# Optimization experiments

Measured on AMD Instinct MI355X. Metric: run time of the kernel, lower is better.

The kernel has to match this reference:

```python
import jax, jax.numpy as jnp
import numpy as np

I, H, O = 3, 16, 5
B, S = 4096, 512


def setup_inputs() -> dict:
    key = jax.random.key(0)
    ks = jax.random.split(key, 4)
    scale = 0.1  # xavier gain=0.1 ballpark; exact init irrelevant for correctness baseline
    return {
        "x": jax.random.normal(ks[0], (B, S, I), dtype=jnp.float32),
        "W_ih": jax.random.normal(ks[1], (4 * H, I), dtype=jnp.float32) * scale,
        "W_hh": jax.random.normal(ks[2], (4 * H, H), dtype=jnp.float32) * scale,
        "b_ih": jnp.zeros((4 * H,), dtype=jnp.float32),
        "b_hh": jnp.zeros((4 * H,), dtype=jnp.float32),
        "W_lin": jax.random.normal(ks[3], (O, H), dtype=jnp.float32) * scale,
        "b_lin": jnp.zeros((O,), dtype=jnp.float32),
    }


def _lstm(x, W_ih, W_hh, b_ih, b_hh):
    # Precompute input contribution for all timesteps: [B, S, 4H]
    xg = jnp.einsum('bsi,gi->bsg', x, W_ih) + b_ih + b_hh
    xg = jnp.swapaxes(xg, 0, 1)  # [S, B, 4H] for scan
    h0 = jnp.zeros((x.shape[0], H), dtype=x.dtype)
    c0 = jnp.zeros_like(h0)

    def step(carry, xt):
        h, c = carry
        gates = xt + h @ W_hh.T  # [B, 4H]
        i, f, g, o = jnp.split(gates, 4, axis=-1)  # PyTorch gate order i,f,g,o
        i = jax.nn.sigmoid(i)
        f = jax.nn.sigmoid(f)
        g = jnp.tanh(g)
        o = jax.nn.sigmoid(o)
        c = f * c + i * g
        h = o * jnp.tanh(c)
        return (h, c), h

    _, hs = jax.lax.scan(step, (h0, c0), xg)
    return jnp.swapaxes(hs, 0, 1)  # [B, S, H]


def reference(x, W_ih, W_hh, b_ih, b_hh, W_lin, b_lin):
    out1 = _lstm(x, W_ih, W_hh, b_ih, b_hh)            # [B, S, H]
    out = jnp.einsum('bsh,oh->bso', out1, W_lin) + b_lin  # [B, S, O]
    return jnp.clip(out, -10.0, 10.0)
```

## Files before the change

### kernel.cpp

```cpp
#include <hip/hip_runtime.h>


#define TS 512
#define LOG2E 1.44269504088896340736f

typedef float f32x2 __attribute__((ext_vector_type(2)));

#define BCAST(K) hbr[K] = __int_as_float( \
    __builtin_amdgcn_update_dpp(0, hvi, 0x150 + (K), 0xf, 0xf, true))
#define BCAST_ALL() \
  BCAST(0); BCAST(1); BCAST(2); BCAST(3); BCAST(4); BCAST(5); BCAST(6); BCAST(7); \
  BCAST(8); BCAST(9); BCAST(10); BCAST(11); BCAST(12); BCAST(13); BCAST(14); BCAST(15)

__global__ __launch_bounds__(256)
__attribute__((amdgpu_waves_per_eu(1, 1)))
void lstm_enc_kernel(const float* __restrict__ x,
                     const float* __restrict__ W_ih,
                     const float* __restrict__ W_hh,
                     const float* __restrict__ b_ih,
                     const float* __restrict__ b_hh,
                     const float* __restrict__ W_lin,
                     const float* __restrict__ b_lin,
                     float* __restrict__ out) {
  const int tid = threadIdx.x;
  const int j = tid & 15;
  const int g = tid >> 4;
  const int batch = blockIdx.x * 16 + g;
  const int jo = (j < 5) ? j : 0;

  __shared__ float4 xs[2][64][16];
  float4* xsf = &xs[0][0][0];

  f32x2 wif[16], wgo[16];
  float wl[16];
#pragma unroll
  for (int k = 0; k < 16; ++k) {
    wif[k] = f32x2{W_hh[(j     ) * 16 + k] * LOG2E,
                   W_hh[(j + 16) * 16 + k] * LOG2E};
    wgo[k] = f32x2{W_hh[(j + 32) * 16 + k] * (2.0f * LOG2E),
                   W_hh[(j + 48) * 16 + k] * LOG2E};
    wl[k]  = W_lin[jo * 16 + k];
  }
  f32x2 xw[3], xwg[3];
#pragma unroll
  for (int i = 0; i < 3; ++i) {
    xw[i]  = f32x2{W_ih[(j     ) * 3 + i] * LOG2E,
                   W_ih[(j + 16) * 3 + i] * LOG2E};
    xwg[i] = f32x2{W_ih[(j + 32) * 3 + i] * (2.0f * LOG2E),
                   W_ih[(j + 48) * 3 + i] * LOG2E};
  }
  const f32x2 bif = f32x2{(b_ih[j     ] + b_hh[j     ]) * LOG2E,
                          (b_ih[j + 16] + b_hh[j + 16]) * LOG2E};
  const f32x2 bgo = f32x2{(b_ih[j + 32] + b_hh[j + 32]) * (2.0f * LOG2E),
                          (b_ih[j + 48] + b_hh[j + 48]) * LOG2E};
  const float bl = b_lin[jo];

  const float* __restrict__ xb = x + (size_t)batch * (TS * 3);
  float* __restrict__ ob = out + (size_t)batch * (TS * 5) + j;
  const bool storer = (j < 5);

  const float* xc0 = xb + j * 12;
  float4 q0, q1, q2;

  q0 = *(const float4*)(xc0 + 0);
  q1 = *(const float4*)(xc0 + 4);
  q2 = *(const float4*)(xc0 + 8);
  {
    const int wb = j * 4 * 16 + g;
    xsf[wb +  0] = float4{q0.x, q0.y, q0.z, 0.f};
    xsf[wb + 16] = float4{q0.w, q1.x, q1.y, 0.f};
    xsf[wb + 32] = float4{q1.z, q1.w, q2.x, 0.f};
    xsf[wb + 48] = float4{q2.y, q2.z, q2.w, 0.f};
  }
  q0 = *(const float4*)(xc0 + 192 + 0);
  q1 = *(const float4*)(xc0 + 192 + 4);
  q2 = *(const float4*)(xc0 + 192 + 8);

  float4 xr[2];
  xr[0] = xsf[0 * 16 + g];
  xr[1] = xsf[1 * 16 + g];

  float h = 0.0f, c = 0.0f;

  auto step = [&](int s, int slot) {
    const float4 xt = xr[slot];
    xr[slot] = xsf[(((s + 2) & 127) << 4) + g];

    float hbr[16];
    const int hvi = __float_as_int(h);
    BCAST_ALL();

    f32x2 aa = bif, ab = f32x2{0.f, 0.f};
    f32x2 ga = bgo, gb = f32x2{0.f, 0.f};
    float oa0 = bl, oa1 = 0.f;
    aa = f32x2{xt.x, xt.x} * xw[0] + aa;
    ab = f32x2{xt.y, xt.y} * xw[1] + ab;
    aa = f32x2{xt.z, xt.z} * xw[2] + aa;
    ga = f32x2{xt.x, xt.x} * xwg[0] + ga;
    gb = f32x2{xt.y, xt.y} * xwg[1] + gb;
    ga = f32x2{xt.z, xt.z} * xwg[2] + ga;
#pragma unroll
    for (int k = 0; k < 16; k += 2) {
      const f32x2 h0 = f32x2{hbr[k], hbr[k]};
      const f32x2 h1 = f32x2{hbr[k + 1], hbr[k + 1]};
      aa = h0 * wif[k] + aa;
      ab = h1 * wif[k + 1] + ab;
      ga = h0 * wgo[k] + ga;
      gb = h1 * wgo[k + 1] + gb;
      oa0 = fmaf(hbr[k], wl[k], oa0);
      oa1 = fmaf(hbr[k + 1], wl[k + 1], oa1);
    }
    const f32x2 zif = aa + ab;
    const f32x2 zgo = ga + gb;

    if (s > 0 && storer) {
      const float oa = oa0 + oa1;
      ob[(s - 1) * 5] = fminf(fmaxf(oa, -10.0f), 10.0f);
    }

    const float ig = __builtin_amdgcn_rcpf(1.0f + __builtin_amdgcn_exp2f(-zif.x));
    const float fg = __builtin_amdgcn_rcpf(1.0f + __builtin_amdgcn_exp2f(-zif.y));
    const float sg = __builtin_amdgcn_rcpf(1.0f + __builtin_amdgcn_exp2f(zgo.x));
    const float og = __builtin_amdgcn_rcpf(1.0f + __builtin_amdgcn_exp2f(-zgo.y));

    const float gg = fmaf(-2.0f, sg, 1.0f);
    c = fmaf(fg, c, ig * gg);
    const float tc = fmaf(-2.0f,
        __builtin_amdgcn_rcpf(1.0f + __builtin_amdgcn_exp2f((2.0f * LOG2E) * c)), 1.0f);
    h = og * tc;
  };

  for (int ch = 0; ch < 8; ++ch) {
    const int base = ch * 64;

#pragma unroll 2
    for (int u = 0; u < 32; ++u) step(base + u, u & 1);

    if (ch < 7) {
      const int p = (ch + 1) & 1;
      const int wb = p * 1024 + j * 64 + g;
      xsf[wb +  0] = float4{q0.x, q0.y, q0.z, 0.f};
      xsf[wb + 16] = float4{q0.w, q1.x, q1.y, 0.f};
      xsf[wb + 32] = float4{q1.z, q1.w, q2.x, 0.f};
      xsf[wb + 48] = float4{q2.y, q2.z, q2.w, 0.f};
    }
    if (ch < 6) {
      const float* xc = xc0 + (ch + 2) * 192;
      q0 = *(const float4*)(xc + 0);
      q1 = *(const float4*)(xc + 4);
      q2 = *(const float4*)(xc + 8);
    }

#pragma unroll 2
    for (int u = 32; u < 64; ++u) step(base + u, u & 1);
  }

  {
    float hbr[16];
    const int hvi = __float_as_int(h);
    BCAST_ALL();
    float oa = bl;
#pragma unroll
    for (int k = 0; k < 16; ++k) oa = fmaf(hbr[k], wl[k], oa);
    if (storer) {
      ob[(TS - 1) * 5] = fminf(fmaxf(oa, -10.0f), 10.0f);
    }
  }
}

extern "C" void kernel_launch(void* const* d_in, const int* in_sizes, int n_in,
                              void* d_out, int out_size, void* d_ws, size_t ws_size,
                              hipStream_t stream) {
  const float* x     = (const float*)d_in[0];
  const float* W_ih  = (const float*)d_in[1];
  const float* W_hh  = (const float*)d_in[2];
  const float* b_ih  = (const float*)d_in[3];
  const float* b_hh  = (const float*)d_in[4];
  const float* W_lin = (const float*)d_in[5];
  const float* b_lin = (const float*)d_in[6];
  float* out = (float*)d_out;

  const int B = in_sizes[0] / (TS * 3);
  const int grid = B / 16;
  lstm_enc_kernel<<<grid, 256, 0, stream>>>(x, W_ih, W_hh, b_ih, b_hh, W_lin, b_lin, out);
}
```

Baseline: 212.5 us.

## Compute LSTM recurrent gates with split-bf16 MFMA instead of DPP-broadcast FMAs

Replaces the per-lane DPP broadcast of h and scalar packed FMAs with 16x16x32 bf16 MFMA instructions. Each weight and activation is split into hi and lo bf16 parts and three MFMA passes approximate fp32 accuracy. The input projection and the output linear layer are folded into the same matrix product by appending x to the K dimension. Gate results and h are exchanged through per-wave LDS buffers each step. This adds LDS round trips and MFMA latency to the serial recurrence critical path, and precision is only roughly fp32.

```diff
diff --git a/kernel.cpp b/kernel.cpp
--- a/kernel.cpp
+++ b/kernel.cpp
@@ -4,13 +4,15 @@
 #define TS 512
 #define LOG2E 1.44269504088896340736f
 
-typedef float f32x2 __attribute__((ext_vector_type(2)));
-
-#define BCAST(K) hbr[K] = __int_as_float( \
-    __builtin_amdgcn_update_dpp(0, hvi, 0x150 + (K), 0xf, 0xf, true))
-#define BCAST_ALL() \
-  BCAST(0); BCAST(1); BCAST(2); BCAST(3); BCAST(4); BCAST(5); BCAST(6); BCAST(7); \
-  BCAST(8); BCAST(9); BCAST(10); BCAST(11); BCAST(12); BCAST(13); BCAST(14); BCAST(15)
+typedef float f32x4 __attribute__((ext_vector_type(4)));
+typedef short s16x8 __attribute__((ext_vector_type(8)));
+typedef unsigned int u32;
+typedef u32 u32x4 __attribute__((ext_vector_type(4)));
+typedef f32x4 f32x4u __attribute__((aligned(4)));
+
+static __device__ __forceinline__ float clip10(float v) {
+  return fminf(fmaxf(v, -10.0f), 10.0f);
+}
 
 __global__ __launch_bounds__(256)
 __attribute__((amdgpu_waves_per_eu(1, 1)))
@@ -23,147 +25,231 @@
                      const float* __restrict__ b_lin,
                      float* __restrict__ out) {
   const int tid = threadIdx.x;
-  const int j = tid & 15;
-  const int g = tid >> 4;
-  const int batch = blockIdx.x * 16 + g;
-  const int jo = (j < 5) ? j : 0;
+  const int w   = tid >> 6;
+  const int q   = (tid >> 4) & 3;
+  const int col = tid & 15;
+  const int g16 = tid >> 4;
 
   __shared__ float4 xs[2][64][16];
+  __shared__ f32x4  zbuf[4][4][20];
+  __shared__ __attribute__((aligned(16))) u32 hbuf[4][4][36];
+
   float4* xsf = &xs[0][0][0];
-
-  f32x2 wif[16], wgo[16];
-  float wl[16];
-#pragma unroll
-  for (int k = 0; k < 16; ++k) {
-    wif[k] = f32x2{W_hh[(j     ) * 16 + k] * LOG2E,
-                   W_hh[(j + 16) * 16 + k] * LOG2E};
-    wgo[k] = f32x2{W_hh[(j + 32) * 16 + k] * (2.0f * LOG2E),
-                   W_hh[(j + 48) * 16 + k] * LOG2E};
-    wl[k]  = W_lin[jo * 16 + k];
-  }
-  f32x2 xw[3], xwg[3];
-#pragma unroll
-  for (int i = 0; i < 3; ++i) {
-    xw[i]  = f32x2{W_ih[(j     ) * 3 + i] * LOG2E,
-                   W_ih[(j + 16) * 3 + i] * LOG2E};
-    xwg[i] = f32x2{W_ih[(j + 32) * 3 + i] * (2.0f * LOG2E),
-                   W_ih[(j + 48) * 3 + i] * LOG2E};
-  }
-  const f32x2 bif = f32x2{(b_ih[j     ] + b_hh[j     ]) * LOG2E,
-                          (b_ih[j + 16] + b_hh[j + 16]) * LOG2E};
-  const f32x2 bgo = f32x2{(b_ih[j + 32] + b_hh[j + 32]) * (2.0f * LOG2E),
-                          (b_ih[j + 48] + b_hh[j + 48]) * LOG2E};
-  const float bl = b_lin[jo];
-
-  const float* __restrict__ xb = x + (size_t)batch * (TS * 3);
-  float* __restrict__ ob = out + (size_t)batch * (TS * 5) + j;
-  const bool storer = (j < 5);
-
-  const float* xc0 = xb + j * 12;
-  float4 q0, q1, q2;
-
-  q0 = *(const float4*)(xc0 + 0);
-  q1 = *(const float4*)(xc0 + 4);
-  q2 = *(const float4*)(xc0 + 8);
+  float*  zf  = (float*)&zbuf[w][0][0];
+  u32*    hb  = &hbuf[w][0][0];
+
+  s16x8 a_hi[4], a_lo[4];
+#pragma unroll
+  for (int G = 0; G < 4; ++G) {
+    const float sc = (G == 2) ? (2.0f * LOG2E) : LOG2E;
+#pragma unroll
+    for (int e = 0; e < 8; ++e) {
+      const int k = q * 8 + e;
+      float v = 0.0f;
+      if (k < 16)      v = W_hh[(G * 16 + col) * 16 + k] * sc;
+      else if (k < 19) v = W_ih[(G * 16 + col) * 3 + (k - 16)] * sc;
+      const u32 vb = __float_as_uint(v);
+      const float hif = __uint_as_float(vb & 0xFFFF0000u);
+      const float lof = v - hif;
+      a_hi[G][e] = (short)(vb >> 16);
+      a_lo[G][e] = (short)(__float_as_uint(lof) >> 16);
+    }
+  }
+  s16x8 l_hi, l_lo;
+#pragma unroll
+  for (int e = 0; e < 8; ++e) {
+    const int k = q * 8 + e;
+    const float v = (col < 5 && k < 16) ? W_lin[col * 16 + k] : 0.0f;
+    const u32 vb = __float_as_uint(v);
+    const float hif = __uint_as_float(vb & 0xFFFF0000u);
+    const float lof = v - hif;
+    l_hi[e] = (short)(vb >> 16);
+    l_lo[e] = (short)(__float_as_uint(lof) >> 16);
+  }
+  f32x4 bias_c[4];
+#pragma unroll
+  for (int G = 0; G < 4; ++G) {
+    const float sc = (G == 2) ? (2.0f * LOG2E) : LOG2E;
+#pragma unroll
+    for (int r = 0; r < 4; ++r)
+      bias_c[G][r] = (b_ih[G * 16 + q * 4 + r] + b_hh[G * 16 + q * 4 + r]) * sc;
+  }
+  f32x4 blin_c;
+#pragma unroll
+  for (int r = 0; r < 4; ++r) {
+    const int row = q * 4 + r;
+    blin_c[r] = (row < 5) ? b_lin[row] : 0.0f;
+  }
+
+  const int batch_g = blockIdx.x * 16 + g16;
+  const float* __restrict__ xb = x + (size_t)batch_g * (TS * 3);
+  const float* xc0 = xb + col * 12;
+  float4 p0, p1, p2;
+  p0 = *(const float4*)(xc0 + 0);
+  p1 = *(const float4*)(xc0 + 4);
+  p2 = *(const float4*)(xc0 + 8);
   {
-    const int wb = j * 4 * 16 + g;
-    xsf[wb +  0] = float4{q0.x, q0.y, q0.z, 0.f};
-    xsf[wb + 16] = float4{q0.w, q1.x, q1.y, 0.f};
-    xsf[wb + 32] = float4{q1.z, q1.w, q2.x, 0.f};
-    xsf[wb + 48] = float4{q2.y, q2.z, q2.w, 0.f};
-  }
-  q0 = *(const float4*)(xc0 + 192 + 0);
-  q1 = *(const float4*)(xc0 + 192 + 4);
-  q2 = *(const float4*)(xc0 + 192 + 8);
-
-  float4 xr[2];
-  xr[0] = xsf[0 * 16 + g];
-  xr[1] = xsf[1 * 16 + g];
-
-  float h = 0.0f, c = 0.0f;
-
-  auto step = [&](int s, int slot) {
-    const float4 xt = xr[slot];
-    xr[slot] = xsf[(((s + 2) & 127) << 4) + g];
-
-    float hbr[16];
-    const int hvi = __float_as_int(h);
-    BCAST_ALL();
-
-    f32x2 aa = bif, ab = f32x2{0.f, 0.f};
-    f32x2 ga = bgo, gb = f32x2{0.f, 0.f};
-    float oa0 = bl, oa1 = 0.f;
-    aa = f32x2{xt.x, xt.x} * xw[0] + aa;
-    ab = f32x2{xt.y, xt.y} * xw[1] + ab;
-    aa = f32x2{xt.z, xt.z} * xw[2] + aa;
-    ga = f32x2{xt.x, xt.x} * xwg[0] + ga;
-    gb = f32x2{xt.y, xt.y} * xwg[1] + gb;
-    ga = f32x2{xt.z, xt.z} * xwg[2] + ga;
-#pragma unroll
-    for (int k = 0; k < 16; k += 2) {
-      const f32x2 h0 = f32x2{hbr[k], hbr[k]};
-      const f32x2 h1 = f32x2{hbr[k + 1], hbr[k + 1]};
-      aa = h0 * wif[k] + aa;
-      ab = h1 * wif[k + 1] + ab;
-      ga = h0 * wgo[k] + ga;
-      gb = h1 * wgo[k + 1] + gb;
-      oa0 = fmaf(hbr[k], wl[k], oa0);
-      oa1 = fmaf(hbr[k + 1], wl[k + 1], oa1);
-    }
-    const f32x2 zif = aa + ab;
-    const f32x2 zgo = ga + gb;
-
-    if (s > 0 && storer) {
-      const float oa = oa0 + oa1;
-      ob[(s - 1) * 5] = fminf(fmaxf(oa, -10.0f), 10.0f);
-    }
-
-    const float ig = __builtin_amdgcn_rcpf(1.0f + __builtin_amdgcn_exp2f(-zif.x));
-    const float fg = __builtin_amdgcn_rcpf(1.0f + __builtin_amdgcn_exp2f(-zif.y));
-    const float sg = __builtin_amdgcn_rcpf(1.0f + __builtin_amdgcn_exp2f(zgo.x));
-    const float og = __builtin_amdgcn_rcpf(1.0f + __builtin_amdgcn_exp2f(-zgo.y));
-
+    const int wb = col * 64 + g16;
+    xsf[wb +  0] = float4{p0.x, p0.y, p0.z, 0.f};
+    xsf[wb + 16] = float4{p0.w, p1.x, p1.y, 0.f};
+    xsf[wb + 32] = float4{p1.z, p1.w, p2.x, 0.f};
+    xsf[wb + 48] = float4{p2.y, p2.z, p2.w, 0.f};
+  }
+  p0 = *(const float4*)(xc0 + 192 + 0);
+  p1 = *(const float4*)(xc0 + 192 + 4);
+  p2 = *(const float4*)(xc0 + 192 + 8);
+
+  {
+    const int l = tid & 63;
+#pragma unroll
+    for (int i = 0; i < 3; ++i) {
+      const int idx = l + i * 64;
+      if (idx < 144) hb[idx] = 0;
+    }
+    const float4 xt0 = xsf[g16];
+    const float xv = (col == 0) ? xt0.x : ((col == 1) ? xt0.y : xt0.z);
+    if (col < 3) {
+      const u32 xbits = __float_as_uint(xv);
+      const float xhi = __uint_as_float(xbits & 0xFFFF0000u);
+      const float xlo = xv - xhi;
+      hb[q * 36 + 16 + col] = __builtin_amdgcn_perm(xbits, __float_as_uint(xlo), 0x07060302u);
+    }
+  }
+
+  float* __restrict__ ob = out + (size_t)(blockIdx.x * 16 + w * 4 + (col & 3)) * (TS * 5);
+  float c = 0.0f;
+
+  auto step = [&](int s) {
+    const float4 xt = xsf[(((s + 1) & 127) << 4) + g16];
+
+    const int hoff = (col & 3) * 36 + q * 8;
+    const u32x4 d0 = *(const u32x4*)&hb[hoff];
+    const u32x4 d1 = *(const u32x4*)&hb[hoff + 4];
+    u32x4 hi4, lo4;
+    hi4.x = __builtin_amdgcn_perm(d0.y, d0.x, 0x07060302u);
+    lo4.x = __builtin_amdgcn_perm(d0.y, d0.x, 0x05040100u);
+    hi4.y = __builtin_amdgcn_perm(d0.w, d0.z, 0x07060302u);
+    lo4.y = __builtin_amdgcn_perm(d0.w, d0.z, 0x05040100u);
+    hi4.z = __builtin_amdgcn_perm(d1.y, d1.x, 0x07060302u);
+    lo4.z = __builtin_amdgcn_perm(d1.y, d1.x, 0x05040100u);
+    hi4.w = __builtin_amdgcn_perm(d1.w, d1.z, 0x07060302u);
+    lo4.w = __builtin_amdgcn_perm(d1.w, d1.z, 0x05040100u);
+    const s16x8 Bhi = __builtin_bit_cast(s16x8, hi4);
+    const s16x8 Blo = __builtin_bit_cast(s16x8, lo4);
+
+    f32x4 z0 = __builtin_amdgcn_mfma_f32_16x16x32_bf16(a_lo[0], Bhi, bias_c[0], 0, 0, 0);
+    f32x4 z1 = __builtin_amdgcn_mfma_f32_16x16x32_bf16(a_lo[1], Bhi, bias_c[1], 0, 0, 0);
+    f32x4 z2 = __builtin_amdgcn_mfma_f32_16x16x32_bf16(a_lo[2], Bhi, bias_c[2], 0, 0, 0);
+    f32x4 z3 = __builtin_amdgcn_mfma_f32_16x16x32_bf16(a_lo[3], Bhi, bias_c[3], 0, 0, 0);
+    f32x4 ov = __builtin_amdgcn_mfma_f32_16x16x32_bf16(l_lo,    Bhi, blin_c,    0, 0, 0);
+    z0 = __builtin_amdgcn_mfma_f32_16x16x32_bf16(a_hi[0], Blo, z0, 0, 0, 0);
+    z1 = __builtin_amdgcn_mfma_f32_16x16x32_bf16(a_hi[1], Blo, z1, 0, 0, 0);
+    z2 = __builtin_amdgcn_mfma_f32_16x16x32_bf16(a_hi[2], Blo, z2, 0, 0, 0);
+    z3 = __builtin_amdgcn_mfma_f32_16x16x32_bf16(a_hi[3], Blo, z3, 0, 0, 0);
+    ov = __builtin_amdgcn_mfma_f32_16x16x32_bf16(l_hi,    Blo, ov, 0, 0, 0);
+    z0 = __builtin_amdgcn_mfma_f32_16x16x32_bf16(a_hi[0], Bhi, z0, 0, 0, 0);
+    z1 = __builtin_amdgcn_mfma_f32_16x16x32_bf16(a_hi[1], Bhi, z1, 0, 0, 0);
+    z2 = __builtin_amdgcn_mfma_f32_16x16x32_bf16(a_hi[2], Bhi, z2, 0, 0, 0);
+    z3 = __builtin_amdgcn_mfma_f32_16x16x32_bf16(a_hi[3], Bhi, z3, 0, 0, 0);
+    ov = __builtin_amdgcn_mfma_f32_16x16x32_bf16(l_hi,    Bhi, ov, 0, 0, 0);
+
+    if (col < 4) {
+      zbuf[w][col][0 * 4 + q] = z0;
+      zbuf[w][col][1 * 4 + q] = z1;
+      zbuf[w][col][2 * 4 + q] = z2;
+      zbuf[w][col][3 * 4 + q] = z3;
+    }
+
+    if (s > 0 && col < 4) {
+      if (q == 0) {
+        f32x4 o;
+        o.x = clip10(ov.x); o.y = clip10(ov.y); o.z = clip10(ov.z); o.w = clip10(ov.w);
+        *(f32x4u*)(ob + (s - 1) * 5) = o;
+      } else if (q == 1) {
+        ob[(s - 1) * 5 + 4] = clip10(ov.x);
+      }
+    }
+
+    const int zo_ = q * 80 + col;
+    const float zi  = zf[zo_ +  0];
+    const float zfg = zf[zo_ + 16];
+    const float zg  = zf[zo_ + 32];
+    const float zo  = zf[zo_ + 48];
+
+    const float ig = __builtin_amdgcn_rcpf(1.0f + __builtin_amdgcn_exp2f(-zi));
+    const float fg = __builtin_amdgcn_rcpf(1.0f + __builtin_amdgcn_exp2f(-zfg));
+    const float sg = __builtin_amdgcn_rcpf(1.0f + __builtin_amdgcn_exp2f(zg));
+    const float og = __builtin_amdgcn_rcpf(1.0f + __builtin_amdgcn_exp2f(-zo));
     const float gg = fmaf(-2.0f, sg, 1.0f);
     c = fmaf(fg, c, ig * gg);
     const float tc = fmaf(-2.0f,
         __builtin_amdgcn_rcpf(1.0f + __builtin_amdgcn_exp2f((2.0f * LOG2E) * c)), 1.0f);
-    h = og * tc;
+    const float h = og * tc;
+
+    const u32 hbits = __float_as_uint(h);
+    const float hhi = __uint_as_float(hbits & 0xFFFF0000u);
+    const float hlo = h - hhi;
+    hb[q * 36 + col] = __builtin_amdgcn_perm(hbits, __float_as_uint(hlo), 0x07060302u);
+
+    const float xv = (col == 0) ? xt.x : ((col == 1) ? xt.y : xt.z);
+    if (col < 3) {
+      const u32 xbits = __float_as_uint(xv);
+      const float xhi = __uint_as_float(xbits & 0xFFFF0000u);
+      const float xlo = xv - xhi;
+      hb[q * 36 + 16 + col] = __builtin_amdgcn_perm(xbits, __float_as_uint(xlo), 0x07060302u);
+    }
   };
 
   for (int ch = 0; ch < 8; ++ch) {
     const int base = ch * 64;
-
 #pragma unroll 2
-    for (int u = 0; u < 32; ++u) step(base + u, u & 1);
+    for (int u = 0; u < 32; ++u) step(base + u);
 
     if (ch < 7) {
       const int p = (ch + 1) & 1;
-      const int wb = p * 1024 + j * 64 + g;
-      xsf[wb +  0] = float4{q0.x, q0.y, q0.z, 0.f};
-      xsf[wb + 16] = float4{q0.w, q1.x, q1.y, 0.f};
-      xsf[wb + 32] = float4{q1.z, q1.w, q2.x, 0.f};
-      xsf[wb + 48] = float4{q2.y, q2.z, q2.w, 0.f};
+      const int wb = p * 1024 + col * 64 + g16;
+      xsf[wb +  0] = float4{p0.x, p0.y, p0.z, 0.f};
+      xsf[wb + 16] = float4{p0.w, p1.x, p1.y, 0.f};
+      xsf[wb + 32] = float4{p1.z, p1.w, p2.x, 0.f};
+      xsf[wb + 48] = float4{p2.y, p2.z, p2.w, 0.f};
     }
     if (ch < 6) {
       const float* xc = xc0 + (ch + 2) * 192;
-      q0 = *(const float4*)(xc + 0);
-      q1 = *(const float4*)(xc + 4);
-      q2 = *(const float4*)(xc + 8);
+      p0 = *(const float4*)(xc + 0);
+      p1 = *(const float4*)(xc + 4);
+      p2 = *(const float4*)(xc + 8);
     }
 
 #pragma unroll 2
-    for (int u = 32; u < 64; ++u) step(base + u, u & 1);
+    for (int u = 32; u < 64; ++u) step(base + u);
   }
 
   {
-    float hbr[16];
-    const int hvi = __float_as_int(h);
-    BCAST_ALL();
-    float oa = bl;
-#pragma unroll
-    for (int k = 0; k < 16; ++k) oa = fmaf(hbr[k], wl[k], oa);
-    if (storer) {
-      ob[(TS - 1) * 5] = fminf(fmaxf(oa, -10.0f), 10.0f);
+    const int hoff = (col & 3) * 36 + q * 8;
+    const u32x4 d0 = *(const u32x4*)&hb[hoff];
+    const u32x4 d1 = *(const u32x4*)&hb[hoff + 4];
+    u32x4 hi4, lo4;
+    hi4.x = __builtin_amdgcn_perm(d0.y, d0.x, 0x07060302u);
+    lo4.x = __builtin_amdgcn_perm(d0.y, d0.x, 0x05040100u);
+    hi4.y = __builtin_amdgcn_perm(d0.w, d0.z, 0x07060302u);
+    lo4.y = __builtin_amdgcn_perm(d0.w, d0.z, 0x05040100u);
+    hi4.z = __builtin_amdgcn_perm(d1.y, d1.x, 0x07060302u);
+    lo4.z = __builtin_amdgcn_perm(d1.y, d1.x, 0x05040100u);
+    hi4.w = __builtin_amdgcn_perm(d1.w, d1.z, 0x07060302u);
+    lo4.w = __builtin_amdgcn_perm(d1.w, d1.z, 0x05040100u);
+    const s16x8 Bhi = __builtin_bit_cast(s16x8, hi4);
+    const s16x8 Blo = __builtin_bit_cast(s16x8, lo4);
+    f32x4 ov = __builtin_amdgcn_mfma_f32_16x16x32_bf16(l_lo, Bhi, blin_c, 0, 0, 0);
+    ov = __builtin_amdgcn_mfma_f32_16x16x32_bf16(l_hi, Blo, ov, 0, 0, 0);
+    ov = __builtin_amdgcn_mfma_f32_16x16x32_bf16(l_hi, Bhi, ov, 0, 0, 0);
+    if (col < 4) {
+      if (q == 0) {
+        f32x4 o;
+        o.x = clip10(ov.x); o.y = clip10(ov.y); o.z = clip10(ov.z); o.w = clip10(ov.w);
+        *(f32x4u*)(ob + (TS - 1) * 5) = o;
+      } else if (q == 1) {
+        ob[(TS - 1) * 5 + 4] = clip10(ov.x);
+      }
     }
   }
 }
```

After: 315.2 us. 48.3% more time.

## Split each hidden unit's recurrent dot product across two lanes with swizzle reduction

Applied to the files above, without the earlier changes.

Each batch sequence now uses 32 lanes instead of 16. Each half-row of lanes computes the gate partial sums over 8 of the 16 hidden inputs, and the halves are combined with a ds_swizzle cross-half add. This halves the serial FMA and DPP-broadcast chain per timestep, doubles the grid and allows two waves per EU. The cost is extra swizzle latency on the critical path and duplicated activation math in both halves.

```diff
diff --git a/kernel.cpp b/kernel.cpp
--- a/kernel.cpp
+++ b/kernel.cpp
@@ -8,12 +8,15 @@
 
 #define BCAST(K) hbr[K] = __int_as_float( \
     __builtin_amdgcn_update_dpp(0, hvi, 0x150 + (K), 0xf, 0xf, true))
-#define BCAST_ALL() \
-  BCAST(0); BCAST(1); BCAST(2); BCAST(3); BCAST(4); BCAST(5); BCAST(6); BCAST(7); \
-  BCAST(8); BCAST(9); BCAST(10); BCAST(11); BCAST(12); BCAST(13); BCAST(14); BCAST(15)
+#define BCAST8() \
+  BCAST(0); BCAST(1); BCAST(2); BCAST(3); BCAST(4); BCAST(5); BCAST(6); BCAST(7)
+
+static __device__ __forceinline__ float swz16(float v) {
+  return __int_as_float(__builtin_amdgcn_ds_swizzle(__float_as_int(v), 0x401F));
+}
 
 __global__ __launch_bounds__(256)
-__attribute__((amdgpu_waves_per_eu(1, 1)))
+__attribute__((amdgpu_waves_per_eu(2)))
 void lstm_enc_kernel(const float* __restrict__ x,
                      const float* __restrict__ W_ih,
                      const float* __restrict__ W_hh,
@@ -23,72 +26,84 @@
                      const float* __restrict__ b_lin,
                      float* __restrict__ out) {
   const int tid = threadIdx.x;
-  const int j = tid & 15;
-  const int g = tid >> 4;
-  const int batch = blockIdx.x * 16 + g;
-  const int jo = (j < 5) ? j : 0;
-
-  __shared__ float4 xs[2][64][16];
+  const int u   = tid & 15;
+  const int hh  = (tid >> 4) & 1;
+  const int g8  = tid >> 5;
+  const int l32 = tid & 31;
+  const int batch = blockIdx.x * 8 + g8;
+  const int jo = (u < 5) ? u : 0;
+
+  __shared__ float4 xs[2][128][8];
   float4* xsf = &xs[0][0][0];
 
-  f32x2 wif[16], wgo[16];
-  float wl[16];
-#pragma unroll
-  for (int k = 0; k < 16; ++k) {
-    wif[k] = f32x2{W_hh[(j     ) * 16 + k] * LOG2E,
-                   W_hh[(j + 16) * 16 + k] * LOG2E};
-    wgo[k] = f32x2{W_hh[(j + 32) * 16 + k] * (2.0f * LOG2E),
-                   W_hh[(j + 48) * 16 + k] * LOG2E};
-    wl[k]  = W_lin[jo * 16 + k];
+  f32x2 wif[8], wgo[8];
+  float wl[8];
+#pragma unroll
+  for (int e = 0; e < 8; ++e) {
+    const int k = hh * 8 + e;
+    wif[e] = f32x2{W_hh[(u     ) * 16 + k] * LOG2E,
+                   W_hh[(u + 16) * 16 + k] * LOG2E};
+    wgo[e] = f32x2{W_hh[(u + 32) * 16 + k] * (2.0f * LOG2E),
+                   W_hh[(u + 48) * 16 + k] * LOG2E};
+    wl[e]  = W_lin[jo * 16 + k];
   }
   f32x2 xw[3], xwg[3];
 #pragma unroll
   for (int i = 0; i < 3; ++i) {
-    xw[i]  = f32x2{W_ih[(j     ) * 3 + i] * LOG2E,
-                   W_ih[(j + 16) * 3 + i] * LOG2E};
-    xwg[i] = f32x2{W_ih[(j + 32) * 3 + i] * (2.0f * LOG2E),
-                   W_ih[(j + 48) * 3 + i] * LOG2E};
-  }
-  const f32x2 bif = f32x2{(b_ih[j     ] + b_hh[j     ]) * LOG2E,
-                          (b_ih[j + 16] + b_hh[j + 16]) * LOG2E};
-  const f32x2 bgo = f32x2{(b_ih[j + 32] + b_hh[j + 32]) * (2.0f * LOG2E),
-                          (b_ih[j + 48] + b_hh[j + 48]) * LOG2E};
-  const float bl = b_lin[jo];
+    if (hh) {
+      xw[i]  = f32x2{W_ih[(u     ) * 3 + i] * LOG2E,
+                     W_ih[(u + 16) * 3 + i] * LOG2E};
+      xwg[i] = f32x2{W_ih[(u + 32) * 3 + i] * (2.0f * LOG2E),
+                     W_ih[(u + 48) * 3 + i] * LOG2E};
+    } else {
+      xw[i] = f32x2{0.f, 0.f};
+      xwg[i] = f32x2{0.f, 0.f};
+    }
+  }
+  const f32x2 bif = hh ? f32x2{0.f, 0.f}
+                       : f32x2{(b_ih[u     ] + b_hh[u     ]) * LOG2E,
+                               (b_ih[u + 16] + b_hh[u + 16]) * LOG2E};
+  const f32x2 bgo = hh ? f32x2{0.f, 0.f}
+                       : f32x2{(b_ih[u + 32] + b_hh[u + 32]) * (2.0f * LOG2E),
+                               (b_ih[u + 48] + b_hh[u + 48]) * LOG2E};
+  const float bl = hh ? 0.f : b_lin[jo];
 
   const float* __restrict__ xb = x + (size_t)batch * (TS * 3);
-  float* __restrict__ ob = out + (size_t)batch * (TS * 5) + j;
-  const bool storer = (j < 5);
-
-  const float* xc0 = xb + j * 12;
+  float* __restrict__ ob = out + (size_t)batch * (TS * 5) + u;
+  const bool storer = (u < 5) && (hh == 0);
+
+  const float* xc0 = xb + l32 * 12;
   float4 q0, q1, q2;
-
   q0 = *(const float4*)(xc0 + 0);
   q1 = *(const float4*)(xc0 + 4);
   q2 = *(const float4*)(xc0 + 8);
   {
-    const int wb = j * 4 * 16 + g;
+    const int wb = (l32 * 4) * 8 + g8;
     xsf[wb +  0] = float4{q0.x, q0.y, q0.z, 0.f};
-    xsf[wb + 16] = float4{q0.w, q1.x, q1.y, 0.f};
-    xsf[wb + 32] = float4{q1.z, q1.w, q2.x, 0.f};
-    xsf[wb + 48] = float4{q2.y, q2.z, q2.w, 0.f};
-  }
-  q0 = *(const float4*)(xc0 + 192 + 0);
-  q1 = *(const float4*)(xc0 + 192 + 4);
-  q2 = *(const float4*)(xc0 + 192 + 8);
+    xsf[wb +  8] = float4{q0.w, q1.x, q1.y, 0.f};
+    xsf[wb + 16] = float4{q1.z, q1.w, q2.x, 0.f};
+    xsf[wb + 24] = float4{q2.y, q2.z, q2.w, 0.f};
+  }
+  q0 = *(const float4*)(xc0 + 384 + 0);
+  q1 = *(const float4*)(xc0 + 384 + 4);
+  q2 = *(const float4*)(xc0 + 384 + 8);
 
   float4 xr[2];
-  xr[0] = xsf[0 * 16 + g];
-  xr[1] = xsf[1 * 16 + g];
+  xr[0] = xsf[0 * 8 + g8];
+  xr[1] = xsf[1 * 8 + g8];
 
   float h = 0.0f, c = 0.0f;
 
   auto step = [&](int s, int slot) {
     const float4 xt = xr[slot];
-    xr[slot] = xsf[(((s + 2) & 127) << 4) + g];
-
-    float hbr[16];
-    const int hvi = __float_as_int(h);
-    BCAST_ALL();
+    xr[slot] = xsf[(((s + 2) & 255) << 3) + g8];
+
+    const float h_rot = __int_as_float(
+        __builtin_amdgcn_update_dpp(0, __float_as_int(h), 0x128, 0xf, 0xf, true));
+    const float hs = hh ? h_rot : h;
+    const int hvi = __float_as_int(hs);
+    float hbr[8];
+    BCAST8();
 
     f32x2 aa = bif, ab = f32x2{0.f, 0.f};
     f32x2 ga = bgo, gb = f32x2{0.f, 0.f};
@@ -100,28 +115,34 @@
     gb = f32x2{xt.y, xt.y} * xwg[1] + gb;
     ga = f32x2{xt.z, xt.z} * xwg[2] + ga;
 #pragma unroll
-    for (int k = 0; k < 16; k += 2) {
-      const f32x2 h0 = f32x2{hbr[k], hbr[k]};
-      const f32x2 h1 = f32x2{hbr[k + 1], hbr[k + 1]};
-      aa = h0 * wif[k] + aa;
-      ab = h1 * wif[k + 1] + ab;
-      ga = h0 * wgo[k] + ga;
-      gb = h1 * wgo[k + 1] + gb;
-      oa0 = fmaf(hbr[k], wl[k], oa0);
-      oa1 = fmaf(hbr[k + 1], wl[k + 1], oa1);
-    }
-    const f32x2 zif = aa + ab;
-    const f32x2 zgo = ga + gb;
+    for (int e = 0; e < 8; e += 2) {
+      const f32x2 h0 = f32x2{hbr[e], hbr[e]};
+      const f32x2 h1 = f32x2{hbr[e + 1], hbr[e + 1]};
+      aa = h0 * wif[e] + aa;
+      ab = h1 * wif[e + 1] + ab;
+      ga = h0 * wgo[e] + ga;
+      gb = h1 * wgo[e + 1] + gb;
+      oa0 = fmaf(hbr[e], wl[e], oa0);
+      oa1 = fmaf(hbr[e + 1], wl[e + 1], oa1);
+    }
+    const f32x2 zl = aa + ab;
+    const f32x2 gl = ga + gb;
+    const float oal = oa0 + oa1;
+
+    const float zi  = zl.x + swz16(zl.x);
+    const float zfg = zl.y + swz16(zl.y);
+    const float zg  = gl.x + swz16(gl.x);
+    const float zo  = gl.y + swz16(gl.y);
+    const float oa  = oal + swz16(oal);
 
     if (s > 0 && storer) {
-      const float oa = oa0 + oa1;
       ob[(s - 1) * 5] = fminf(fmaxf(oa, -10.0f), 10.0f);
     }
 
-    const float ig = __builtin_amdgcn_rcpf(1.0f + __builtin_amdgcn_exp2f(-zif.x));
-    const float fg = __builtin_amdgcn_rcpf(1.0f + __builtin_amdgcn_exp2f(-zif.y));
-    const float sg = __builtin_amdgcn_rcpf(1.0f + __builtin_amdgcn_exp2f(zgo.x));
-    const float og = __builtin_amdgcn_rcpf(1.0f + __builtin_amdgcn_exp2f(-zgo.y));
+    const float ig = __builtin_amdgcn_rcpf(1.0f + __builtin_amdgcn_exp2f(-zi));
+    const float fg = __builtin_amdgcn_rcpf(1.0f + __builtin_amdgcn_exp2f(-zfg));
+    const float sg = __builtin_amdgcn_rcpf(1.0f + __builtin_amdgcn_exp2f(zg));
+    const float og = __builtin_amdgcn_rcpf(1.0f + __builtin_amdgcn_exp2f(-zo));
 
     const float gg = fmaf(-2.0f, sg, 1.0f);
     c = fmaf(fg, c, ig * gg);
@@ -130,38 +151,46 @@
     h = og * tc;
   };
 
-  for (int ch = 0; ch < 8; ++ch) {
-    const int base = ch * 64;
+  for (int ch = 0; ch < 4; ++ch) {
+    const int base = ch * 128;
 
 #pragma unroll 2
-    for (int u = 0; u < 32; ++u) step(base + u, u & 1);
-
-    if (ch < 7) {
+    for (int v = 0; v < 64; ++v) step(base + v, v & 1);
+
+    if (ch < 3) {
       const int p = (ch + 1) & 1;
-      const int wb = p * 1024 + j * 64 + g;
+      const int wb = (p * 128 + l32 * 4) * 8 + g8;
       xsf[wb +  0] = float4{q0.x, q0.y, q0.z, 0.f};
-      xsf[wb + 16] = float4{q0.w, q1.x, q1.y, 0.f};
-      xsf[wb + 32] = float4{q1.z, q1.w, q2.x, 0.f};
-      xsf[wb + 48] = float4{q2.y, q2.z, q2.w, 0.f};
-    }
-    if (ch < 6) {
-      const float* xc = xc0 + (ch + 2) * 192;
+      xsf[wb +  8] = float4{q0.w, q1.x, q1.y, 0.f};
+      xsf[wb + 16] = float4{q1.z, q1.w, q2.x, 0.f};
+      xsf[wb + 24] = float4{q2.y, q2.z, q2.w, 0.f};
+    }
+    if (ch < 2) {
+      const float* xc = xc0 + (ch + 2) * 384;
       q0 = *(const float4*)(xc + 0);
       q1 = *(const float4*)(xc + 4);
       q2 = *(const float4*)(xc + 8);
     }
 
 #pragma unroll 2
-    for (int u = 32; u < 64; ++u) step(base + u, u & 1);
+    for (int v = 64; v < 128; ++v) step(base + v, v & 1);
   }
 
   {
-    float hbr[16];
-    const int hvi = __float_as_int(h);
-    BCAST_ALL();
-    float oa = bl;
-#pragma unroll
-    for (int k = 0; k < 16; ++k) oa = fmaf(hbr[k], wl[k], oa);
+    const float h_rot = __int_as_float(
+        __builtin_amdgcn_update_dpp(0, __float_as_int(h), 0x128, 0xf, 0xf, true));
+    const float hs = hh ? h_rot : h;
+    const int hvi = __float_as_int(hs);
+    float hbr[8];
+    BCAST8();
+    float oa0 = bl, oa1 = 0.f;
+#pragma unroll
+    for (int e = 0; e < 8; e += 2) {
+      oa0 = fmaf(hbr[e], wl[e], oa0);
+      oa1 = fmaf(hbr[e + 1], wl[e + 1], oa1);
+    }
+    const float oal = oa0 + oa1;
+    const float oa = oal + swz16(oal);
     if (storer) {
       ob[(TS - 1) * 5] = fminf(fmaxf(oa, -10.0f), 10.0f);
     }
@@ -181,6 +210,6 @@
   float* out = (float*)d_out;
 
   const int B = in_sizes[0] / (TS * 3);
-  const int grid = B / 16;
+  const int grid = B / 8;
   lstm_enc_kernel<<<grid, 256, 0, stream>>>(x, W_ih, W_hh, b_ih, b_hh, W_lin, b_lin, out);
 }
```

After: 260.0 us. 1.22x slower.
